# Performance work log

Hardware: AMD Instinct MI355X
Metric: run time of the kernel (lower is better)

The kernel has to match this reference:

```python
import jax, jax.numpy as jnp
import numpy as np

RRELU_SLOPE = (1.0 / 8.0 + 1.0 / 3.0) / 2.0  # RReLU eval-mode negative slope


def _layer(h, edge_feats, src, dst, W, b, Lw, Lb, n_nodes):
    # per-edge message: concat(src node feat, edge feat) -> linear
    msg = jnp.concatenate([h[src], edge_feats], axis=-1) @ W + b  # [E, H]
    # mean-aggregate messages by destination node (0 for isolated nodes, DGL semantics)
    s = jax.ops.segment_sum(msg, dst, num_segments=n_nodes)  # [N, H]
    cnt = jax.ops.segment_sum(jnp.ones((dst.shape[0], 1), msg.dtype), dst,
                              num_segments=n_nodes)  # [N, 1]
    agg = jnp.where(cnt > 0, s / jnp.maximum(cnt, 1.0), 0.0)
    # self-loop linear add
    agg = agg + h @ Lw + Lb
    # RReLU (eval mode = leaky relu with slope (lower+upper)/2); dropout p=0 is identity
    return jnp.where(agg >= 0, agg, agg * RRELU_SLOPE)


def setup_inputs() -> dict:
    key = jax.random.key(0)
    ks = jax.random.split(key, 12)
    N, E, D, H = 50000, 640000, 128, 128
    sc_in = 1.0 / np.sqrt(2 * D)
    sc_d = 1.0 / np.sqrt(D)
    sc_o = 1.0 / np.sqrt(2 * H)
    return {
        "node_feats": jax.random.normal(ks[0], (N, D), jnp.float32),
        "edge_feats": jax.random.normal(ks[1], (E, D), jnp.float32),
        "src": jax.random.randint(ks[2], (E,), 0, N),
        "dst": jax.random.randint(ks[3], (E,), 0, N),
        "W1": jax.random.uniform(ks[4], (2 * D, H), jnp.float32, -sc_in, sc_in),
        "b1": jnp.zeros((H,), jnp.float32),
        "L1": jax.random.uniform(ks[5], (D, H), jnp.float32, -sc_d, sc_d),
        "lb1": jnp.zeros((H,), jnp.float32),
        "W2": jax.random.uniform(ks[6], (2 * H, H), jnp.float32, -sc_in, sc_in),
        "b2": jnp.zeros((H,), jnp.float32),
        "L2": jax.random.uniform(ks[7], (H, H), jnp.float32, -sc_d, sc_d),
        "lb2": jnp.zeros((H,), jnp.float32),
        "Wo": jax.random.uniform(ks[8], (2 * H, H), jnp.float32, -sc_o, sc_o),
        "bo": jnp.zeros((H,), jnp.float32),
    }


def reference(node_feats, edge_feats, src, dst, W1, b1, L1, lb1, W2, b2, L2, lb2, Wo, bo):
    n = node_feats.shape[0]
    h1 = _layer(node_feats, edge_feats, src, dst, W1, b1, L1, lb1, n)
    h2 = _layer(h1, edge_feats, src, dst, W2, b2, L2, lb2, n)
    multihop = jnp.concatenate([h1, h2], axis=-1)  # [N, 2H]
    return multihop @ Wo + bo
```

## Files before the change

### kernel.cpp

```cpp
#include <hip/hip_runtime.h>
#include <hip/hip_bf16.h>

typedef unsigned short u16;
typedef unsigned int   u32;

using bf16x8 = __attribute__((ext_vector_type(8))) __bf16;
using f32x4  = __attribute__((ext_vector_type(4))) float;

#define SLOPE 0.22916666666666666f
#define CAP 64

static __device__ __forceinline__ u16 f2bf(float f) {
    u32 u = __float_as_uint(f);
    u += 0x7fffu + ((u >> 16) & 1u);
    return (u16)(u >> 16);
}
static __device__ __forceinline__ float bf2f(u16 h) {
    return __uint_as_float(((u32)h) << 16);
}

static __device__ __forceinline__ void gload_lds16(const u16* g, u16* l) {
    __builtin_amdgcn_global_load_lds(
        (const __attribute__((address_space(1))) void*)g,
        (__attribute__((address_space(3))) void*)l,
        16, 0, 0);
}

static __device__ __forceinline__ void add8(float* a, uint4 u) {
    a[0] += bf2f((u16)u.x); a[1] += bf2f((u16)(u.x >> 16));
    a[2] += bf2f((u16)u.y); a[3] += bf2f((u16)(u.y >> 16));
    a[4] += bf2f((u16)u.z); a[5] += bf2f((u16)(u.z >> 16));
    a[6] += bf2f((u16)u.w); a[7] += bf2f((u16)(u.w >> 16));
}

__global__ void k_prep(const int* __restrict__ src, const int* __restrict__ dst,
                       int* __restrict__ deg, int2* __restrict__ se,
                       const float* __restrict__ node, u16* __restrict__ nfb,
                       const float* __restrict__ W1, const float* __restrict__ L1,
                       const float* __restrict__ W2, const float* __restrict__ L2,
                       const float* __restrict__ Wo, u16* __restrict__ T,
                       int E, int n8, int gE, int gF) {
    int b = blockIdx.x, t = threadIdx.x;
    if (b < gE) {
        int i = b * 256 + t;
        if (i < E) {
            int d = dst[i];
            int p = atomicAdd(&deg[d], 1);
            if (p < CAP) se[(size_t)d * CAP + p] = make_int2(src[i], i);
        }
    } else if (b < gE + gF) {
        int i = (b - gE) * 256 + t;
        if (i < n8) {
            const float4* p = (const float4*)node + (size_t)i * 2;
            float4 a = p[0], c = p[1];
            union { u16 u[8]; uint4 v; } pk;
            pk.u[0] = f2bf(a.x); pk.u[1] = f2bf(a.y); pk.u[2] = f2bf(a.z); pk.u[3] = f2bf(a.w);
            pk.u[4] = f2bf(c.x); pk.u[5] = f2bf(c.y); pk.u[6] = f2bf(c.z); pk.u[7] = f2bf(c.w);
            *((uint4*)nfb + i) = pk.v;
        }
    } else {
        int m = b - gE - gF;
        const float* S; int rowoff;
        switch (m) {
            case 0: S = W1; rowoff = 0;   break;
            case 1: S = W1; rowoff = 128; break;
            case 2: S = L1; rowoff = 0;   break;
            case 3: S = W2; rowoff = 0;   break;
            case 4: S = W2; rowoff = 128; break;
            case 5: S = L2; rowoff = 0;   break;
            case 6: S = Wo; rowoff = 0;   break;
            default: S = Wo; rowoff = 128; break;
        }
        u16* O = T + m * 16384;
        for (int i = t; i < 16384; i += 256) {
            int c = i >> 7, k = i & 127;
            O[i] = f2bf(S[(rowoff + k) * 128 + c]);
        }
    }
}

__global__ void k_aggf(const float* __restrict__ ef, const u16* __restrict__ nfb,
                       const int2* __restrict__ se, const int* __restrict__ deg,
                       u16* __restrict__ EF, u16* __restrict__ A, int N) {
    int w = (blockIdx.x * blockDim.x + threadIdx.x) >> 6;
    int lane = threadIdx.x & 63;
    if (w >= N) return;
    int t4 = lane >> 4, qq = lane & 15;
    int d = deg[w];
    int dc = d < CAP ? d : CAP;
    const int2* sp = se + (size_t)w * CAP;
    float e[8] = {0.f, 0.f, 0.f, 0.f, 0.f, 0.f, 0.f, 0.f};
    float n[8] = {0.f, 0.f, 0.f, 0.f, 0.f, 0.f, 0.f, 0.f};
    int i = 0;
    for (; i + 8 <= dc; i += 8) {
        int2 iA = sp[i + t4], iB = sp[i + 4 + t4];
        const float* ra = ef + (size_t)iA.y * 128 + qq * 8;
        const float* rb = ef + (size_t)iB.y * 128 + qq * 8;
        float4 a0 = *(const float4*)ra, a1 = *(const float4*)(ra + 4);
        float4 c0 = *(const float4*)rb, c1 = *(const float4*)(rb + 4);
        uint4 ua = *(const uint4*)(nfb + (size_t)iA.x * 128 + qq * 8);
        uint4 ub = *(const uint4*)(nfb + (size_t)iB.x * 128 + qq * 8);
        e[0] += a0.x + c0.x; e[1] += a0.y + c0.y; e[2] += a0.z + c0.z; e[3] += a0.w + c0.w;
        e[4] += a1.x + c1.x; e[5] += a1.y + c1.y; e[6] += a1.z + c1.z; e[7] += a1.w + c1.w;
        add8(n, ua); add8(n, ub);
    }
    for (; i + 4 <= dc; i += 4) {
        int2 iA = sp[i + t4];
        const float* ra = ef + (size_t)iA.y * 128 + qq * 8;
        float4 a0 = *(const float4*)ra, a1 = *(const float4*)(ra + 4);
        uint4 ua = *(const uint4*)(nfb + (size_t)iA.x * 128 + qq * 8);
        e[0] += a0.x; e[1] += a0.y; e[2] += a0.z; e[3] += a0.w;
        e[4] += a1.x; e[5] += a1.y; e[6] += a1.z; e[7] += a1.w;
        add8(n, ua);
    }
    if (i + t4 < dc) {
        int2 iA = sp[i + t4];
        const float* ra = ef + (size_t)iA.y * 128 + qq * 8;
        float4 a0 = *(const float4*)ra, a1 = *(const float4*)(ra + 4);
        uint4 ua = *(const uint4*)(nfb + (size_t)iA.x * 128 + qq * 8);
        e[0] += a0.x; e[1] += a0.y; e[2] += a0.z; e[3] += a0.w;
        e[4] += a1.x; e[5] += a1.y; e[6] += a1.z; e[7] += a1.w;
        add8(n, ua);
    }
    #pragma unroll
    for (int j = 0; j < 8; j++) {
        e[j] += __shfl_xor(e[j], 16); e[j] += __shfl_xor(e[j], 32);
        n[j] += __shfl_xor(n[j], 16); n[j] += __shfl_xor(n[j], 32);
    }
    float sc = d > 0 ? 1.0f / (float)d : 0.0f;
    if (t4 == 0) {
        union { u16 u[8]; uint4 v; } pk;
        #pragma unroll
        for (int j = 0; j < 8; j++) pk.u[j] = f2bf(e[j] * sc);
        *(uint4*)(EF + (size_t)w * 128 + qq * 8) = pk.v;
    } else if (t4 == 1) {
        union { u16 u[8]; uint4 v; } pk;
        #pragma unroll
        for (int j = 0; j < 8; j++) pk.u[j] = f2bf(n[j] * sc);
        *(uint4*)(A + (size_t)w * 128 + qq * 8) = pk.v;
    }
}

__global__ void k_aggb(const u16* __restrict__ h, const int2* __restrict__ se,
                       const int* __restrict__ deg, u16* __restrict__ out, int N) {
    int w = (blockIdx.x * blockDim.x + threadIdx.x) >> 6;
    int lane = threadIdx.x & 63;
    if (w >= N) return;
    int quarter = lane >> 4, q = lane & 15;
    int d = deg[w];
    int dc = d < CAP ? d : CAP;
    const int2* sp = se + (size_t)w * CAP;
    float a[8] = {0.f, 0.f, 0.f, 0.f, 0.f, 0.f, 0.f, 0.f};
    int i = 0;
    for (; i + 8 <= dc; i += 8) {
        int eA = sp[i + quarter].x, eB = sp[i + 4 + quarter].x;
        uint4 uA = *(const uint4*)(h + (size_t)eA * 128 + q * 8);
        uint4 uB = *(const uint4*)(h + (size_t)eB * 128 + q * 8);
        add8(a, uA); add8(a, uB);
    }
    for (; i + 4 <= dc; i += 4) {
        int eA = sp[i + quarter].x;
        uint4 uA = *(const uint4*)(h + (size_t)eA * 128 + q * 8);
        add8(a, uA);
    }
    if (i + quarter < dc) {
        int eA = sp[i + quarter].x;
        uint4 uA = *(const uint4*)(h + (size_t)eA * 128 + q * 8);
        add8(a, uA);
    }
    #pragma unroll
    for (int j = 0; j < 8; j++) {
        a[j] += __shfl_xor(a[j], 32);
        a[j] += __shfl_xor(a[j], 16);
    }
    if (quarter == 0) {
        float sc = d > 0 ? 1.0f / (float)d : 0.0f;
        union { u16 u[8]; uint4 v; } pk;
        #pragma unroll
        for (int j = 0; j < 8; j++) pk.u[j] = f2bf(a[j] * sc);
        *(uint4*)(out + (size_t)w * 128 + q * 8) = pk.v;
    }
}

#define STAGE_X(LBUF, GPTR)                                                         \
    {                                                                               \
        _Pragma("unroll")                                                           \
        for (int i_ = 0; i_ < 4; i_++) {                                            \
            int id_ = t + i_ * 256;                                                 \
            int r_ = id_ >> 4, c16_ = id_ & 15;                                     \
            int rg_ = row0 + r_; if (rg_ >= N) rg_ = N - 1;                         \
            gload_lds16((GPTR) + (size_t)rg_ * 128 + ((c16_ ^ (r_ & 15)) << 3),     \
                        (LBUF) + id_ * 8);                                          \
        }                                                                           \
    }
#define STAGE_W(GPTR)                                                               \
    {                                                                               \
        _Pragma("unroll")                                                           \
        for (int i_ = 0; i_ < 8; i_++) {                                            \
            int id_ = t + i_ * 256;                                                 \
            int cc_ = id_ >> 4, c16_ = id_ & 15;                                    \
            gload_lds16((GPTR) + cc_ * 128 + ((c16_ ^ (cc_ & 15)) << 3),            \
                        Wl + id_ * 8);                                              \
        }                                                                           \
    }
#define COMPUTE(LBUF)                                                               \
    {                                                                               \
        _Pragma("unroll")                                                           \
        for (int ks_ = 0; ks_ < 4; ks_++) {                                         \
            bf16x8 af_[2], bf_[4];                                                  \
            _Pragma("unroll")                                                       \
            for (int h_ = 0; h_ < 2; h_++) {                                        \
                int r_ = wr * 32 + h_ * 16 + lanelo;                                \
                int ch_ = (ks_ * 4 + lanehi) ^ (r_ & 15);                           \
                af_[h_] = *(const bf16x8*)((LBUF) + r_ * 128 + ch_ * 8);            \
            }                                                                       \
            _Pragma("unroll")                                                       \
            for (int g_ = 0; g_ < 4; g_++) {                                        \
                int cc_ = wc * 64 + g_ * 16 + lanelo;                               \
                int ch_ = (ks_ * 4 + lanehi) ^ (cc_ & 15);                          \
                bf_[g_] = *(const bf16x8*)(Wl + cc_ * 128 + ch_ * 8);               \
            }                                                                       \
            _Pragma("unroll")                                                       \
            for (int h_ = 0; h_ < 2; h_++)                                          \
                _Pragma("unroll")                                                   \
                for (int g_ = 0; g_ < 4; g_++)                                      \
                    acc[h_][g_] = __builtin_amdgcn_mfma_f32_16x16x32_bf16(          \
                        af_[h_], bf_[g_], acc[h_][g_], 0, 0, 0);                    \
        }                                                                           \
    }

__global__ __launch_bounds__(256) void k_gemm1(
    const u16* __restrict__ X0, const u16* __restrict__ X1, const u16* __restrict__ X2,
    const u16* __restrict__ T0, const u16* __restrict__ T1, const u16* __restrict__ T2,
    const float* __restrict__ bm, const int* __restrict__ deg,
    const float* __restrict__ ba, u16* __restrict__ outp, int N) {

    __shared__ u16 Xl[64 * 128];
    __shared__ u16 Wl[128 * 128];

    int t = threadIdx.x, lane = t & 63, wid = t >> 6;
    int lanelo = lane & 15, lanehi = lane >> 4;
    int wr = wid >> 1, wc = wid & 1;
    int row0 = blockIdx.x * 64;

    f32x4 acc[2][4];
    #pragma unroll
    for (int h = 0; h < 2; h++)
        #pragma unroll
        for (int g = 0; g < 4; g++) acc[h][g] = (f32x4){0.f, 0.f, 0.f, 0.f};

    const u16* Xs[3] = {X0, X1, X2};
    const u16* Ts[3] = {T0, T1, T2};
    for (int s = 0; s < 3; s++) {
        __syncthreads();
        STAGE_X(Xl, Xs[s]);
        STAGE_W(Ts[s]);
        __syncthreads();
        COMPUTE(Xl);
    }

    #pragma unroll
    for (int h = 0; h < 2; h++) {
        #pragma unroll
        for (int r = 0; r < 4; r++) {
            int rowt = wr * 32 + h * 16 + lanehi * 4 + r;
            int rg = row0 + rowt;
            if (rg >= N) continue;
            float m = (deg[rg] > 0) ? 1.f : 0.f;
            #pragma unroll
            for (int g = 0; g < 4; g++) {
                int col = wc * 64 + g * 16 + lanelo;
                float v = acc[h][g][r] + ba[col] + m * bm[col];
                v = (v >= 0.f) ? v : v * SLOPE;
                outp[(size_t)rg * 128 + col] = f2bf(v);
            }
        }
    }
}

__global__ __launch_bounds__(256) void k_gemm23(
    const u16* __restrict__ A2, const u16* __restrict__ EF, const u16* __restrict__ H1,
    const u16* __restrict__ TW2a, const u16* __restrict__ TW2b, const u16* __restrict__ TL2,
    const u16* __restrict__ TWoA, const u16* __restrict__ TWoB,
    const float* __restrict__ b2, const float* __restrict__ lb2,
    const float* __restrict__ bo, const int* __restrict__ deg,
    float* __restrict__ outp, int N) {

    __shared__ u16 XA[64 * 128];
    __shared__ u16 XE[64 * 128];
    __shared__ u16 XH[64 * 128];
    __shared__ u16 Wl[128 * 128];

    int t = threadIdx.x, lane = t & 63, wid = t >> 6;
    int lanelo = lane & 15, lanehi = lane >> 4;
    int wr = wid >> 1, wc = wid & 1;
    int row0 = blockIdx.x * 64;

    f32x4 acc[2][4];
    #pragma unroll
    for (int h = 0; h < 2; h++)
        #pragma unroll
        for (int g = 0; g < 4; g++) acc[h][g] = (f32x4){0.f, 0.f, 0.f, 0.f};

    STAGE_X(XA, A2);
    STAGE_X(XE, EF);
    STAGE_X(XH, H1);
    STAGE_W(TW2a);
    __syncthreads();
    COMPUTE(XA);
    __syncthreads();
    STAGE_W(TW2b);
    __syncthreads();
    COMPUTE(XE);
    __syncthreads();
    STAGE_W(TL2);
    __syncthreads();
    COMPUTE(XH);

    #pragma unroll
    for (int h = 0; h < 2; h++) {
        #pragma unroll
        for (int r = 0; r < 4; r++) {
            int rowt = wr * 32 + h * 16 + lanehi * 4 + r;
            int rg = row0 + rowt;
            float m = (rg < N && deg[rg] > 0) ? 1.f : 0.f;
            #pragma unroll
            for (int g = 0; g < 4; g++) {
                int col = wc * 64 + g * 16 + lanelo;
                float v = acc[h][g][r] + lb2[col] + m * b2[col];
                v = (v >= 0.f) ? v : v * SLOPE;
                XA[rowt * 128 + ((((col >> 3) ^ (rowt & 15)) << 3) | (col & 7))] = f2bf(v);
                acc[h][g][r] = 0.f;
            }
        }
    }
    __syncthreads();
    STAGE_W(TWoA);
    __syncthreads();
    COMPUTE(XH);
    __syncthreads();
    STAGE_W(TWoB);
    __syncthreads();
    COMPUTE(XA);

    #pragma unroll
    for (int h = 0; h < 2; h++) {
        #pragma unroll
        for (int r = 0; r < 4; r++) {
            int rowt = wr * 32 + h * 16 + lanehi * 4 + r;
            int rg = row0 + rowt;
            if (rg >= N) continue;
            #pragma unroll
            for (int g = 0; g < 4; g++) {
                int col = wc * 64 + g * 16 + lanelo;
                outp[(size_t)rg * 128 + col] = acc[h][g][r] + bo[col];
            }
        }
    }
}


extern "C" void kernel_launch(void* const* d_in, const int* in_sizes, int n_in,
                              void* d_out, int out_size, void* d_ws, size_t ws_size,
                              hipStream_t stream) {
    const float* node = (const float*)d_in[0];
    const float* ef   = (const float*)d_in[1];
    const int*   src  = (const int*)d_in[2];
    const int*   dst  = (const int*)d_in[3];
    const float* W1   = (const float*)d_in[4];
    const float* b1   = (const float*)d_in[5];
    const float* L1   = (const float*)d_in[6];
    const float* lb1  = (const float*)d_in[7];
    const float* W2   = (const float*)d_in[8];
    const float* b2   = (const float*)d_in[9];
    const float* L2   = (const float*)d_in[10];
    const float* lb2  = (const float*)d_in[11];
    const float* Wo   = (const float*)d_in[12];
    const float* bo   = (const float*)d_in[13];
    int N = in_sizes[0] / 128;
    int E = in_sizes[2];

    char* ws = (char*)d_ws;
    size_t o = 0;
    auto alloc = [&](size_t bytes) {
        void* p = ws + o;
        o = (o + bytes + 511) & ~(size_t)511;
        return p;
    };
    int*  deg = (int*)alloc((size_t)N * 4);
    int2* se  = (int2*)alloc((size_t)N * CAP * 8);
    u16*  T   = (u16*)alloc((size_t)8 * 16384 * 2);
    u16*  nfb = (u16*)alloc((size_t)N * 128 * 2);
    u16*  EF  = (u16*)alloc((size_t)N * 128 * 2);
    u16*  A   = (u16*)alloc((size_t)N * 128 * 2);
    u16*  h1  = (u16*)alloc((size_t)N * 128 * 2);

    hipMemsetAsync(deg, 0, (size_t)N * 4, stream);

    int gE = (E + 255) / 256;
    int n8 = N * 128 / 8;
    int gF = (n8 + 255) / 256;
    k_prep<<<gE + gF + 8, 256, 0, stream>>>(src, dst, deg, se, node, nfb,
                                            W1, L1, W2, L2, Wo, T, E, n8, gE, gF);

    int gA = (N + 3) / 4;
    k_aggf<<<gA, 256, 0, stream>>>(ef, nfb, se, deg, EF, A, N);

    int gb = (N + 63) / 64;
    k_gemm1<<<gb, 256, 0, stream>>>(A, EF, nfb, T, T + 16384, T + 2 * 16384,
                                    b1, deg, lb1, h1, N);
    k_aggb<<<gA, 256, 0, stream>>>(h1, se, deg, A, N);
    k_gemm23<<<gb, 256, 0, stream>>>(A, EF, h1,
                                     T + 3 * 16384, T + 4 * 16384, T + 5 * 16384,
                                     T + 6 * 16384, T + 7 * 16384,
                                     b2, lb2, bo, deg, (float*)d_out, N);
}
```

Measured before the change: 210.6 us.

## Read GEMM weight fragments directly from global memory instead of staging in LDS

Removes the shared-memory weight tile and its staging loads in both dense GEMM kernels. MFMA B-fragments are now read straight from the pre-transposed weight buffers in global memory, relying on L1/L2 caching. This cuts LDS use and drops most of the barriers between GEMM stages. Launch bounds now request 4 and 3 blocks per CU, aiming for higher occupancy. The cost is repeated per-wave global (cache) loads of the weights in the inner loop, which may add latency compared with LDS reads.

```diff
diff --git a/kernel.cpp b/kernel.cpp
--- a/kernel.cpp
+++ b/kernel.cpp
@@ -193,17 +193,7 @@
                         (LBUF) + id_ * 8);                                          \
         }                                                                           \
     }
-#define STAGE_W(GPTR)                                                               \
-    {                                                                               \
-        _Pragma("unroll")                                                           \
-        for (int i_ = 0; i_ < 8; i_++) {                                            \
-            int id_ = t + i_ * 256;                                                 \
-            int cc_ = id_ >> 4, c16_ = id_ & 15;                                    \
-            gload_lds16((GPTR) + cc_ * 128 + ((c16_ ^ (cc_ & 15)) << 3),            \
-                        Wl + id_ * 8);                                              \
-        }                                                                           \
-    }
-#define COMPUTE(LBUF)                                                               \
+#define COMPUTE_G(LBUF, TG)                                                         \
     {                                                                               \
         _Pragma("unroll")                                                           \
         for (int ks_ = 0; ks_ < 4; ks_++) {                                         \
@@ -216,9 +206,8 @@
             }                                                                       \
             _Pragma("unroll")                                                       \
             for (int g_ = 0; g_ < 4; g_++) {                                        \
-                int cc_ = wc * 64 + g_ * 16 + lanelo;                               \
-                int ch_ = (ks_ * 4 + lanehi) ^ (cc_ & 15);                          \
-                bf_[g_] = *(const bf16x8*)(Wl + cc_ * 128 + ch_ * 8);               \
+                bf_[g_] = *(const bf16x8*)((TG) + (wc * 64 + g_ * 16 + lanelo) * 128 \
+                                            + ks_ * 32 + lanehi * 8);               \
             }                                                                       \
             _Pragma("unroll")                                                       \
             for (int h_ = 0; h_ < 2; h_++)                                          \
@@ -229,14 +218,14 @@
         }                                                                           \
     }
 
-__global__ __launch_bounds__(256) void k_gemm1(
-    const u16* __restrict__ X0, const u16* __restrict__ X1, const u16* __restrict__ X2,
-    const u16* __restrict__ T0, const u16* __restrict__ T1, const u16* __restrict__ T2,
-    const float* __restrict__ bm, const int* __restrict__ deg,
-    const float* __restrict__ ba, u16* __restrict__ outp, int N) {
-
-    __shared__ u16 Xl[64 * 128];
-    __shared__ u16 Wl[128 * 128];
+__global__ __launch_bounds__(256, 4) void k_gemm1(
+    const u16* __restrict__ A, const u16* __restrict__ EF, const u16* __restrict__ NF,
+    const u16* __restrict__ TW1a, const u16* __restrict__ TW1b, const u16* __restrict__ TL1,
+    const float* __restrict__ b1, const int* __restrict__ deg,
+    const float* __restrict__ lb1, u16* __restrict__ outp, int N) {
+
+    __shared__ u16 XE[64 * 128];
+    __shared__ u16 Xo[64 * 128];
 
     int t = threadIdx.x, lane = t & 63, wid = t >> 6;
     int lanelo = lane & 15, lanehi = lane >> 4;
@@ -249,15 +238,15 @@
         #pragma unroll
         for (int g = 0; g < 4; g++) acc[h][g] = (f32x4){0.f, 0.f, 0.f, 0.f};
 
-    const u16* Xs[3] = {X0, X1, X2};
-    const u16* Ts[3] = {T0, T1, T2};
-    for (int s = 0; s < 3; s++) {
-        __syncthreads();
-        STAGE_X(Xl, Xs[s]);
-        STAGE_W(Ts[s]);
-        __syncthreads();
-        COMPUTE(Xl);
-    }
+    STAGE_X(XE, EF);
+    STAGE_X(Xo, A);
+    __syncthreads();
+    COMPUTE_G(Xo, TW1a);
+    COMPUTE_G(XE, TW1b);
+    __syncthreads();
+    STAGE_X(Xo, NF);
+    __syncthreads();
+    COMPUTE_G(Xo, TL1);
 
     #pragma unroll
     for (int h = 0; h < 2; h++) {
@@ -270,7 +259,7 @@
             #pragma unroll
             for (int g = 0; g < 4; g++) {
                 int col = wc * 64 + g * 16 + lanelo;
-                float v = acc[h][g][r] + ba[col] + m * bm[col];
+                float v = acc[h][g][r] + lb1[col] + m * b1[col];
                 v = (v >= 0.f) ? v : v * SLOPE;
                 outp[(size_t)rg * 128 + col] = f2bf(v);
             }
@@ -278,8 +267,8 @@
     }
 }
 
-__global__ __launch_bounds__(256) void k_gemm23(
-    const u16* __restrict__ A2, const u16* __restrict__ EF, const u16* __restrict__ H1,
+__global__ __launch_bounds__(256, 3) void k_gemm2o(
+    const u16* __restrict__ A2, const u16* __restrict__ EFg, const u16* __restrict__ H1,
     const u16* __restrict__ TW2a, const u16* __restrict__ TW2b, const u16* __restrict__ TL2,
     const u16* __restrict__ TWoA, const u16* __restrict__ TWoB,
     const float* __restrict__ b2, const float* __restrict__ lb2,
@@ -289,7 +278,6 @@
     __shared__ u16 XA[64 * 128];
     __shared__ u16 XE[64 * 128];
     __shared__ u16 XH[64 * 128];
-    __shared__ u16 Wl[128 * 128];
 
     int t = threadIdx.x, lane = t & 63, wid = t >> 6;
     int lanelo = lane & 15, lanehi = lane >> 4;
@@ -303,19 +291,12 @@
         for (int g = 0; g < 4; g++) acc[h][g] = (f32x4){0.f, 0.f, 0.f, 0.f};
 
     STAGE_X(XA, A2);
-    STAGE_X(XE, EF);
+    STAGE_X(XE, EFg);
     STAGE_X(XH, H1);
-    STAGE_W(TW2a);
-    __syncthreads();
-    COMPUTE(XA);
-    __syncthreads();
-    STAGE_W(TW2b);
-    __syncthreads();
-    COMPUTE(XE);
-    __syncthreads();
-    STAGE_W(TL2);
-    __syncthreads();
-    COMPUTE(XH);
+    __syncthreads();
+    COMPUTE_G(XA, TW2a);
+    COMPUTE_G(XE, TW2b);
+    COMPUTE_G(XH, TL2);
 
     #pragma unroll
     for (int h = 0; h < 2; h++) {
@@ -335,13 +316,8 @@
         }
     }
     __syncthreads();
-    STAGE_W(TWoA);
-    __syncthreads();
-    COMPUTE(XH);
-    __syncthreads();
-    STAGE_W(TWoB);
-    __syncthreads();
-    COMPUTE(XA);
+    COMPUTE_G(XH, TWoA);
+    COMPUTE_G(XA, TWoB);
 
     #pragma unroll
     for (int h = 0; h < 2; h++) {
@@ -410,7 +386,7 @@
     k_gemm1<<<gb, 256, 0, stream>>>(A, EF, nfb, T, T + 16384, T + 2 * 16384,
                                     b1, deg, lb1, h1, N);
     k_aggb<<<gA, 256, 0, stream>>>(h1, se, deg, A, N);
-    k_gemm23<<<gb, 256, 0, stream>>>(A, EF, h1,
+    k_gemm2o<<<gb, 256, 0, stream>>>(A, EF, h1,
                                      T + 3 * 16384, T + 4 * 16384, T + 5 * 16384,
                                      T + 6 * 16384, T + 7 * 16384,
                                      b2, lb2, bo, deg, (float*)d_out, N);
```

Result: slower. 245.6 us (+16.6%).

## Widen GEMM blocks to 128 rows with 512 threads and single staging buffer

Applied to the files above, without the earlier changes.

Both node GEMM kernels now run 512-thread blocks that each cover 128 rows, so every staged 128x128 weight tile is shared by twice as many rows. The second kernel replaces its three separate input LDS buffers with one buffer that is restaged per operand. It keeps the layer-2 activations packed in registers and writes them back into LDS only after the first output GEMM has consumed the h1 tile. This halves weight traffic per row and trims LDS usage, at the cost of serializing input staging with compute and using larger blocks, which may lower occupancy.

```diff
diff --git a/kernel.cpp b/kernel.cpp
--- a/kernel.cpp
+++ b/kernel.cpp
@@ -182,22 +182,22 @@
     }
 }
 
-#define STAGE_X(LBUF, GPTR)                                                         \
+#define STAGE_X128(LBUF, GPTR)                                                      \
     {                                                                               \
         _Pragma("unroll")                                                           \
         for (int i_ = 0; i_ < 4; i_++) {                                            \
-            int id_ = t + i_ * 256;                                                 \
+            int id_ = t + i_ * 512;                                                 \
             int r_ = id_ >> 4, c16_ = id_ & 15;                                     \
             int rg_ = row0 + r_; if (rg_ >= N) rg_ = N - 1;                         \
             gload_lds16((GPTR) + (size_t)rg_ * 128 + ((c16_ ^ (r_ & 15)) << 3),     \
                         (LBUF) + id_ * 8);                                          \
         }                                                                           \
     }
-#define STAGE_W(GPTR)                                                               \
+#define STAGE_W512(GPTR)                                                            \
     {                                                                               \
         _Pragma("unroll")                                                           \
-        for (int i_ = 0; i_ < 8; i_++) {                                            \
-            int id_ = t + i_ * 256;                                                 \
+        for (int i_ = 0; i_ < 4; i_++) {                                            \
+            int id_ = t + i_ * 512;                                                 \
             int cc_ = id_ >> 4, c16_ = id_ & 15;                                    \
             gload_lds16((GPTR) + cc_ * 128 + ((c16_ ^ (cc_ & 15)) << 3),            \
                         Wl + id_ * 8);                                              \
@@ -229,19 +229,19 @@
         }                                                                           \
     }
 
-__global__ __launch_bounds__(256) void k_gemm1(
-    const u16* __restrict__ X0, const u16* __restrict__ X1, const u16* __restrict__ X2,
-    const u16* __restrict__ T0, const u16* __restrict__ T1, const u16* __restrict__ T2,
-    const float* __restrict__ bm, const int* __restrict__ deg,
-    const float* __restrict__ ba, u16* __restrict__ outp, int N) {
-
-    __shared__ u16 Xl[64 * 128];
+__global__ __launch_bounds__(512, 4) void k_gemm1(
+    const u16* __restrict__ A, const u16* __restrict__ EF, const u16* __restrict__ NF,
+    const u16* __restrict__ TW1a, const u16* __restrict__ TW1b, const u16* __restrict__ TL1,
+    const float* __restrict__ b1, const int* __restrict__ deg,
+    const float* __restrict__ lb1, u16* __restrict__ outp, int N) {
+
+    __shared__ u16 XB[128 * 128];
     __shared__ u16 Wl[128 * 128];
 
     int t = threadIdx.x, lane = t & 63, wid = t >> 6;
     int lanelo = lane & 15, lanehi = lane >> 4;
     int wr = wid >> 1, wc = wid & 1;
-    int row0 = blockIdx.x * 64;
+    int row0 = blockIdx.x * 128;
 
     f32x4 acc[2][4];
     #pragma unroll
@@ -249,15 +249,20 @@
         #pragma unroll
         for (int g = 0; g < 4; g++) acc[h][g] = (f32x4){0.f, 0.f, 0.f, 0.f};
 
-    const u16* Xs[3] = {X0, X1, X2};
-    const u16* Ts[3] = {T0, T1, T2};
-    for (int s = 0; s < 3; s++) {
-        __syncthreads();
-        STAGE_X(Xl, Xs[s]);
-        STAGE_W(Ts[s]);
-        __syncthreads();
-        COMPUTE(Xl);
-    }
+    STAGE_X128(XB, A);
+    STAGE_W512(TW1a);
+    __syncthreads();
+    COMPUTE(XB);
+    __syncthreads();
+    STAGE_X128(XB, EF);
+    STAGE_W512(TW1b);
+    __syncthreads();
+    COMPUTE(XB);
+    __syncthreads();
+    STAGE_X128(XB, NF);
+    STAGE_W512(TL1);
+    __syncthreads();
+    COMPUTE(XB);
 
     #pragma unroll
     for (int h = 0; h < 2; h++) {
@@ -270,7 +275,7 @@
             #pragma unroll
             for (int g = 0; g < 4; g++) {
                 int col = wc * 64 + g * 16 + lanelo;
-                float v = acc[h][g][r] + ba[col] + m * bm[col];
+                float v = acc[h][g][r] + lb1[col] + m * b1[col];
                 v = (v >= 0.f) ? v : v * SLOPE;
                 outp[(size_t)rg * 128 + col] = f2bf(v);
             }
@@ -278,23 +283,21 @@
     }
 }
 
-__global__ __launch_bounds__(256) void k_gemm23(
-    const u16* __restrict__ A2, const u16* __restrict__ EF, const u16* __restrict__ H1,
+__global__ __launch_bounds__(512, 4) void k_gemm2o(
+    const u16* __restrict__ A2, const u16* __restrict__ EFg, const u16* __restrict__ H1,
     const u16* __restrict__ TW2a, const u16* __restrict__ TW2b, const u16* __restrict__ TL2,
     const u16* __restrict__ TWoA, const u16* __restrict__ TWoB,
     const float* __restrict__ b2, const float* __restrict__ lb2,
     const float* __restrict__ bo, const int* __restrict__ deg,
     float* __restrict__ outp, int N) {
 
-    __shared__ u16 XA[64 * 128];
-    __shared__ u16 XE[64 * 128];
-    __shared__ u16 XH[64 * 128];
+    __shared__ u16 XB[128 * 128];
     __shared__ u16 Wl[128 * 128];
 
     int t = threadIdx.x, lane = t & 63, wid = t >> 6;
     int lanelo = lane & 15, lanehi = lane >> 4;
     int wr = wid >> 1, wc = wid & 1;
-    int row0 = blockIdx.x * 64;
+    int row0 = blockIdx.x * 128;
 
     f32x4 acc[2][4];
     #pragma unroll
@@ -302,46 +305,62 @@
         #pragma unroll
         for (int g = 0; g < 4; g++) acc[h][g] = (f32x4){0.f, 0.f, 0.f, 0.f};
 
-    STAGE_X(XA, A2);
-    STAGE_X(XE, EF);
-    STAGE_X(XH, H1);
-    STAGE_W(TW2a);
-    __syncthreads();
-    COMPUTE(XA);
-    __syncthreads();
-    STAGE_W(TW2b);
-    __syncthreads();
-    COMPUTE(XE);
-    __syncthreads();
-    STAGE_W(TL2);
-    __syncthreads();
-    COMPUTE(XH);
-
+    STAGE_X128(XB, A2);
+    STAGE_W512(TW2a);
+    __syncthreads();
+    COMPUTE(XB);
+    __syncthreads();
+    STAGE_X128(XB, EFg);
+    STAGE_W512(TW2b);
+    __syncthreads();
+    COMPUTE(XB);
+    __syncthreads();
+    STAGE_X128(XB, H1);
+    STAGE_W512(TL2);
+    __syncthreads();
+    COMPUTE(XB);
+
+    u32 h2p[2][4][2];
     #pragma unroll
     for (int h = 0; h < 2; h++) {
         #pragma unroll
-        for (int r = 0; r < 4; r++) {
-            int rowt = wr * 32 + h * 16 + lanehi * 4 + r;
-            int rg = row0 + rowt;
-            float m = (rg < N && deg[rg] > 0) ? 1.f : 0.f;
+        for (int g = 0; g < 4; g++) {
+            int col = wc * 64 + g * 16 + lanelo;
+            float vv[4];
             #pragma unroll
-            for (int g = 0; g < 4; g++) {
-                int col = wc * 64 + g * 16 + lanelo;
+            for (int r = 0; r < 4; r++) {
+                int rowt = wr * 32 + h * 16 + lanehi * 4 + r;
+                int rg = row0 + rowt;
+                float m = (rg < N && deg[rg] > 0) ? 1.f : 0.f;
                 float v = acc[h][g][r] + lb2[col] + m * b2[col];
-                v = (v >= 0.f) ? v : v * SLOPE;
-                XA[rowt * 128 + ((((col >> 3) ^ (rowt & 15)) << 3) | (col & 7))] = f2bf(v);
+                vv[r] = (v >= 0.f) ? v : v * SLOPE;
                 acc[h][g][r] = 0.f;
             }
-        }
-    }
-    __syncthreads();
-    STAGE_W(TWoA);
-    __syncthreads();
-    COMPUTE(XH);
-    __syncthreads();
-    STAGE_W(TWoB);
-    __syncthreads();
-    COMPUTE(XA);
+            h2p[h][g][0] = (u32)f2bf(vv[0]) | ((u32)f2bf(vv[1]) << 16);
+            h2p[h][g][1] = (u32)f2bf(vv[2]) | ((u32)f2bf(vv[3]) << 16);
+        }
+    }
+    __syncthreads();
+    STAGE_W512(TWoA);
+    __syncthreads();
+    COMPUTE(XB);
+    __syncthreads();
+    #pragma unroll
+    for (int h = 0; h < 2; h++) {
+        #pragma unroll
+        for (int g = 0; g < 4; g++) {
+            int col = wc * 64 + g * 16 + lanelo;
+            #pragma unroll
+            for (int r = 0; r < 4; r++) {
+                int rowt = wr * 32 + h * 16 + lanehi * 4 + r;
+                u16 hv = (u16)(h2p[h][g][r >> 1] >> ((r & 1) * 16));
+                XB[rowt * 128 + ((((col >> 3) ^ (rowt & 15)) << 3) | (col & 7))] = hv;
+            }
+        }
+    }
+    STAGE_W512(TWoB);
+    __syncthreads();
+    COMPUTE(XB);
 
     #pragma unroll
     for (int h = 0; h < 2; h++) {
@@ -406,11 +425,11 @@
     int gA = (N + 3) / 4;
     k_aggf<<<gA, 256, 0, stream>>>(ef, nfb, se, deg, EF, A, N);
 
-    int gb = (N + 63) / 64;
-    k_gemm1<<<gb, 256, 0, stream>>>(A, EF, nfb, T, T + 16384, T + 2 * 16384,
+    int gb = (N + 127) / 128;
+    k_gemm1<<<gb, 512, 0, stream>>>(A, EF, nfb, T, T + 16384, T + 2 * 16384,
                                     b1, deg, lb1, h1, N);
     k_aggb<<<gA, 256, 0, stream>>>(h1, se, deg, A, N);
-    k_gemm23<<<gb, 256, 0, stream>>>(A, EF, h1,
+    k_gemm2o<<<gb, 512, 0, stream>>>(A, EF, h1,
                                      T + 3 * 16384, T + 4 * 16384, T + 5 * 16384,
                                      T + 6 * 16384, T + 7 * 16384,
                                      b2, lb2, bo, deg, (float*)d_out, N);
```

Result: no change. 211.9 us (+0.6%).
